# Kernel optimization log

Measured on AMD Instinct MI355X. Metric: run time of the kernel, lower is better.

The kernel has to match this reference:

```python
import jax, jax.numpy as jnp
import numpy as np

NUM_GROUPS = 32
EPS = 1e-5


def _conv(x, w, b, pad):
    # x: [B,C,H,W], w: [O,I,kh,kw]
    y = jax.lax.conv_general_dilated(
        x, w, window_strides=(1, 1), padding=[(pad, pad), (pad, pad)],
        dimension_numbers=('NCHW', 'OIHW', 'NCHW'))
    return y + b[None, :, None, None]


def _group_norm(x, gamma, beta):
    B, C, H, W = x.shape
    g = x.reshape(B, NUM_GROUPS, C // NUM_GROUPS, H, W)
    mu = g.mean(axis=(2, 3, 4), keepdims=True)
    var = g.var(axis=(2, 3, 4), keepdims=True)
    g = (g - mu) * jax.lax.rsqrt(var + EPS)
    x = g.reshape(B, C, H, W)
    return x * gamma[None, :, None, None] + beta[None, :, None, None]


def setup_inputs() -> dict:
    key = jax.random.key(0)
    ks = jax.random.split(key, 8)
    B, C, H, W = 8, 384, 64, 64
    s1 = 1.0 / np.sqrt(C)          # 1x1 conv fan-in
    s3 = 1.0 / np.sqrt(C * 9)      # 3x3 conv fan-in
    return {
        'x': jax.random.normal(ks[0], (B, C, H, W), dtype=jnp.float32),
        'gamma': jnp.ones((C,), dtype=jnp.float32),
        'beta': jnp.zeros((C,), dtype=jnp.float32),
        'wq': jax.random.normal(ks[1], (C, C, 1, 1), dtype=jnp.float32) * s1,
        'bq': jnp.zeros((C,), dtype=jnp.float32),
        'wk': jax.random.normal(ks[2], (C, C, 3, 3), dtype=jnp.float32) * s3,
        'bk': jnp.zeros((C,), dtype=jnp.float32),
        'wv': jax.random.normal(ks[3], (C, C, 1, 1), dtype=jnp.float32) * s1,
        'bv': jnp.zeros((C,), dtype=jnp.float32),
        'wf': jax.random.normal(ks[4], (C, C, 1, 1), dtype=jnp.float32) * s1,
        'bf': jnp.zeros((C,), dtype=jnp.float32),
        'k': 512,
    }


def reference(x, gamma, beta, wq, bq, wk, bk, wv, bv, wf, bf, k):
    B, C, H, W = x.shape
    xn = _group_norm(x, gamma, beta)
    q = _conv(xn, wq, bq, 0)
    kk = _conv(xn, wk, bk, 1)
    v = _conv(xn, wv, bv, 0)
    # frequency-domain correlation: elementwise product of 2D spectra
    Fq = jnp.fft.fft2(q)
    Fk = jnp.fft.fft2(kk)
    A = jnp.fft.ifft2(Fq * Fk).real          # [B,C,H,W]
    # per-(batch,channel) spatial top-k sparsification
    A_flat = A.reshape(B, C, H * W)
    topv, _ = jax.lax.top_k(A_flat, k)
    thresh = topv[..., -1:]                   # k-th largest value
    masked = jnp.where(A_flat >= thresh, A_flat, -jnp.inf)
    Fw = jax.nn.softmax(masked, axis=-1).reshape(B, C, H, W)
    F4 = v * Fw                               # weighted values
    res = _conv(F4, wf, bf, 0)
    return xn * res
```

## Files before the change

### kernel.cpp

```cpp
#include <hip/hip_runtime.h>
#include <hip/hip_fp16.h>
#include <math.h>

#define CCH  384
#define BATCH 8
#define HWN  4096
#define NG   32
#define CPG  12
#define KSEL 512
#define FFTP 65
#define LP   40

typedef short v8s  __attribute__((ext_vector_type(8)));
typedef float v16f __attribute__((ext_vector_type(16)));

#define MFMA_B16(A_,B_,C_) __builtin_amdgcn_mfma_f32_32x32x16_bf16((A_),(B_),(C_),0,0,0)

#define BARRIER_NODRAIN() asm volatile("s_waitcnt lgkmcnt(0)\n\ts_barrier" ::: "memory")
#define BARRIER_RAW() asm volatile("s_barrier" ::: "memory")

__device__ __forceinline__ v8s as_v8s(uint4 u) {
  union { uint4 u4; v8s v; } c; c.u4 = u; return c.v;
}
__device__ __forceinline__ unsigned br6(unsigned i) {
  return ((i&1u)<<5)|((i&2u)<<3)|((i&4u)<<1)|((i&8u)>>1)|((i&16u)>>3)|((i&32u)>>5);
}
__device__ __forceinline__ unsigned f2key(float f) {
  unsigned u = __float_as_uint(f);
  return (u & 0x80000000u) ? ~u : (u | 0x80000000u);
}
__device__ __forceinline__ float wave_max(float v) {
#pragma unroll
  for (int o = 32; o > 0; o >>= 1) v = fmaxf(v, __shfl_down(v, o, 64));
  return v;
}
__device__ __forceinline__ float wave_sum(float v) {
#pragma unroll
  for (int o = 32; o > 0; o >>= 1) v += __shfl_down(v, o, 64);
  return v;
}
__device__ __forceinline__ unsigned short bf16_rne(float f) {
  unsigned u = __float_as_uint(f);
  return (unsigned short)((u + 0x7fffu + ((u >> 16) & 1u)) >> 16);
}
__device__ __forceinline__ float bf2f(unsigned short h) {
  return __uint_as_float(((unsigned)h) << 16);
}

#define MFMA12_RR(a0h,a0l,a1h,a1l,b0h,b0l,b1h,b1l)            \
  __builtin_amdgcn_s_setprio(1);                              \
  acc[0][0] = MFMA_B16(a0h, b0h, acc[0][0]);                  \
  acc[0][1] = MFMA_B16(a0h, b1h, acc[0][1]);                  \
  acc[1][0] = MFMA_B16(a1h, b0h, acc[1][0]);                  \
  acc[1][1] = MFMA_B16(a1h, b1h, acc[1][1]);                  \
  acc[0][0] = MFMA_B16(a0h, b0l, acc[0][0]);                  \
  acc[0][1] = MFMA_B16(a0h, b1l, acc[0][1]);                  \
  acc[1][0] = MFMA_B16(a1h, b0l, acc[1][0]);                  \
  acc[1][1] = MFMA_B16(a1h, b1l, acc[1][1]);                  \
  acc[0][0] = MFMA_B16(a0l, b0h, acc[0][0]);                  \
  acc[0][1] = MFMA_B16(a0l, b1h, acc[0][1]);                  \
  acc[1][0] = MFMA_B16(a1l, b0h, acc[1][0]);                  \
  acc[1][1] = MFMA_B16(a1l, b1h, acc[1][1]);                  \
  __builtin_amdgcn_s_setprio(0);

__global__ __launch_bounds__(256) void stats_kernel(const float* __restrict__ x,
                                                    float2* __restrict__ gs,
                                                    unsigned short* __restrict__ zp) {
  int b = blockIdx.x >> 5, g = blockIdx.x & 31;
  if (blockIdx.x == 0 && threadIdx.x < 8) zp[threadIdx.x] = 0;
  size_t base = ((size_t)b * CCH + (size_t)g * CPG) * HWN;
  const float4* xp = (const float4*)(x + base);
  int tid = threadIdx.x;
  const int N4 = CPG * HWN / 4;
  float s = 0.f, ss = 0.f;
  for (int i = tid; i < N4; i += 256) {
    float4 v = xp[i];
    s  += (v.x + v.y) + (v.z + v.w);
    ss += (v.x*v.x + v.y*v.y) + (v.z*v.z + v.w*v.w);
  }
  s = wave_sum(s); ss = wave_sum(ss);
  __shared__ float sb[4], qb[4];
  if ((tid & 63) == 0) { sb[tid >> 6] = s; qb[tid >> 6] = ss; }
  __syncthreads();
  if (tid == 0) {
    float S = sb[0]+sb[1]+sb[2]+sb[3], Q = qb[0]+qb[1]+qb[2]+qb[3];
    float inv = 1.0f / (float)(CPG * HWN);
    float mu = S * inv;
    float var = Q * inv - mu * mu;
    gs[blockIdx.x] = make_float2(mu, rsqrtf(var + 1e-5f));
  }
}

__global__ __launch_bounds__(256) void pack_split_k(const float* __restrict__ w,
    unsigned short* __restrict__ hi, unsigned short* __restrict__ lo, int n) {
  int i = blockIdx.x * 256 + threadIdx.x;
  if (i >= n) return;
  float f = w[i];
  int m = i / 384, ci = i - m * 384;
  int kc = ci >> 4, tt = ci & 15;
  int mb = m >> 5, lm2 = m & 31;
  int l = ((tt >> 3) << 5) | lm2;
  int j = tt & 7;
  size_t o = (((size_t)kc * 12 + mb) << 9) + ((size_t)l << 3) + j;
  unsigned short h = bf16_rne(f);
  hi[o] = h;
  lo[o] = bf16_rne(f - bf2f(h));
}
__global__ __launch_bounds__(256) void pack9_k(const float* __restrict__ w,
    unsigned short* __restrict__ hi, unsigned short* __restrict__ lo) {
  int i = blockIdx.x * 256 + threadIdx.x;
  int r = blockIdx.y;
  float f = w[(size_t)i * 9 + r];
  int m = i / 384, ci = i - m * 384;
  int kc = ci >> 4, tt = ci & 15;
  int mb = m >> 5, lm2 = m & 31;
  int l = ((tt >> 3) << 5) | lm2;
  int j = tt & 7;
  size_t o = (((size_t)(r * 24 + kc) * 12 + mb) << 9) + ((size_t)l << 3) + j;
  unsigned short h = bf16_rne(f);
  hi[o] = h;
  lo[o] = bf16_rne(f - bf2f(h));
}

template<int FUSE, int SPLIT>
__global__ __launch_bounds__(256) void trans_kernel(const float* __restrict__ in,
    const float2* __restrict__ gs, const float* __restrict__ gamma,
    const float* __restrict__ beta,
    unsigned short* __restrict__ oh, unsigned short* __restrict__ ol) {
  __shared__ float ts[64][65];
  int tid = threadIdx.x;
  int b = blockIdx.z, c0 = blockIdx.y * 64, p0 = blockIdx.x * 64;
#pragma unroll
  for (int i = 0; i < 4; ++i) {
    int idx = tid + (i << 8);
    int row = idx >> 4, col = (idx & 15) << 2;
    float4 v = *(const float4*)&in[((size_t)b*CCH + c0 + row)*HWN + p0 + col];
    if (FUSE) {
      int c = c0 + row;
      float2 st = gs[(b << 5) + c / CPG];
      float a = gamma[c] * st.y, bb = beta[c] - st.x * a;
      v.x = v.x*a+bb; v.y = v.y*a+bb; v.z = v.z*a+bb; v.w = v.w*a+bb;
    }
    ts[row][col] = v.x; ts[row][col+1] = v.y; ts[row][col+2] = v.z; ts[row][col+3] = v.w;
  }
  __syncthreads();
#pragma unroll
  for (int i = 0; i < 2; ++i) {
    int idx = tid + (i << 8);
    int p = idx >> 3, cgp = (idx & 7) << 3;
    unsigned short h8[8] __attribute__((aligned(16)));
    unsigned short l8[8] __attribute__((aligned(16)));
#pragma unroll
    for (int j = 0; j < 8; ++j) {
      float f = ts[cgp + j][p];
      unsigned short hb = bf16_rne(f);
      h8[j] = hb;
      if (SPLIT) l8[j] = bf16_rne(f - bf2f(hb));
    }
    size_t o = ((size_t)b*HWN + p0 + p)*CCH + c0 + cgp;
    *(uint4*)&oh[o] = *(const uint4*)h8;
    if (SPLIT) *(uint4*)&ol[o] = *(const uint4*)l8;
  }
}

template<int TAPS, int OUT>
__global__ __launch_bounds__(256, 3) void mm_kernel(
    const unsigned short* __restrict__ Ahg, const unsigned short* __restrict__ Alg,
    const float* __restrict__ bias,
    const unsigned short* __restrict__ Bhg, const unsigned short* __restrict__ Blg,
    const unsigned short* __restrict__ xnTh, const unsigned short* __restrict__ xnTl,
    void* __restrict__ Yv) {
  __shared__ unsigned short Bh_s[2][128*LP], Bl_s[2][128*LP];
  int tid = threadIdx.x;
  int b = blockIdx.z, m0 = blockIdx.y * 128, n0 = blockIdx.x * 128;
  int y0 = blockIdx.x * 2;
  int u0row = tid >> 2, cg = tid & 3;
  int lds0 = u0row * LP + cg * 8, lds1 = lds0 + 64 * LP;
  int lane = tid & 63, wm = tid >> 7, wn = (tid >> 6) & 1;
  int lm = lane & 31, lh = lane >> 5;
  int brow = (wn * 64 + lm) * LP;
  int mbb = blockIdx.y * 4 + wm * 2;
  int laneoff = lane << 3;

  v16f acc[2][2];
#pragma unroll
  for (int t = 0; t < 2; ++t)
#pragma unroll
    for (int s = 0; s < 2; ++s)
#pragma unroll
      for (int g = 0; g < 16; ++g) acc[t][s][g] = 0.f;

  const int NS = TAPS * 12;
  uint4 rb0h, rb0l, rb1h, rb1l;
  uint4 rA0h_h0, rA0l_h0, rA1h_h0, rA1l_h0;
  uint4 rA0h_h1, rA0l_h1, rA1h_h1, rA1l_h1;

  auto issueB = [&](int s) {
    int c0 = s * 32;
    int px = u0row;
    int py0 = y0, py1 = py0 + 1;
    size_t boff0 = ((size_t)b * HWN + py0 * 64 + px) * CCH + cg * 8 + c0;
    size_t boff1 = ((size_t)b * HWN + py1 * 64 + px) * CCH + cg * 8 + c0;
    rb0h = *(const uint4*)(Bhg + boff0);
    rb0l = *(const uint4*)(Blg + boff0);
    rb1h = *(const uint4*)(Bhg + boff1);
    rb1l = *(const uint4*)(Blg + boff1);
  };
  auto loadA0 = [&](int s) {
    int fragcol = s * 2;
    size_t off = (((size_t)fragcol * 12 + mbb) << 9) + laneoff;
    rA0h_h0 = *(const uint4*)(Ahg + off);
    rA0l_h0 = *(const uint4*)(Alg + off);
    rA1h_h0 = *(const uint4*)(Ahg + off + 512);
    rA1l_h0 = *(const uint4*)(Alg + off + 512);
  };
  auto loadA1 = [&](int s) {
    int fragcol = s * 2 + 1;
    size_t off = (((size_t)fragcol * 12 + mbb) << 9) + laneoff;
    rA0h_h1 = *(const uint4*)(Ahg + off);
    rA0l_h1 = *(const uint4*)(Alg + off);
    rA1h_h1 = *(const uint4*)(Ahg + off + 512);
    rA1l_h1 = *(const uint4*)(Alg + off + 512);
  };

  issueB(0);
  loadA0(0); loadA1(0);
  *(uint4*)&Bh_s[0][lds0] = rb0h; *(uint4*)&Bl_s[0][lds0] = rb0l;
  *(uint4*)&Bh_s[0][lds1] = rb1h; *(uint4*)&Bl_s[0][lds1] = rb1l;
  issueB(1);
  BARRIER_NODRAIN();

  for (int s = 0; s < NS; ++s) {
    const int cur = s & 1;
    const unsigned short* Bh = &Bh_s[cur][0];
    const unsigned short* Bl = &Bl_s[cur][0];
    {
      int co = lh << 3;
      v8s b0h = *(const v8s*)&Bh[brow + co];
      v8s b0l = *(const v8s*)&Bl[brow + co];
      v8s b1h = *(const v8s*)&Bh[brow + 32*LP + co];
      v8s b1l = *(const v8s*)&Bl[brow + 32*LP + co];
      v8s a0h = as_v8s(rA0h_h0), a0l = as_v8s(rA0l_h0);
      v8s a1h = as_v8s(rA1h_h0), a1l = as_v8s(rA1l_h0);
      MFMA12_RR(a0h, a0l, a1h, a1l, b0h, b0l, b1h, b1l)
    }
    if (s + 1 < NS) loadA0(s + 1);
    {
      int co = 16 + (lh << 3);
      v8s b0h = *(const v8s*)&Bh[brow + co];
      v8s b0l = *(const v8s*)&Bl[brow + co];
      v8s b1h = *(const v8s*)&Bh[brow + 32*LP + co];
      v8s b1l = *(const v8s*)&Bl[brow + 32*LP + co];
      v8s a0h = as_v8s(rA0h_h1), a0l = as_v8s(rA0l_h1);
      v8s a1h = as_v8s(rA1h_h1), a1l = as_v8s(rA1l_h1);
      MFMA12_RR(a0h, a0l, a1h, a1l, b0h, b0l, b1h, b1l)
    }
    if (s + 1 < NS) {
      loadA1(s + 1);
      int nxt = cur ^ 1;
      *(uint4*)&Bh_s[nxt][lds0] = rb0h; *(uint4*)&Bl_s[nxt][lds0] = rb0l;
      *(uint4*)&Bh_s[nxt][lds1] = rb1h; *(uint4*)&Bl_s[nxt][lds1] = rb1l;
      if (s + 2 < NS) issueB(s + 2);
      BARRIER_NODRAIN();
    }
  }
#pragma unroll
  for (int t = 0; t < 2; ++t) {
    int mb = m0 + wm * 64 + t * 32;
#pragma unroll
    for (int s = 0; s < 2; ++s) {
      int n = n0 + wn * 64 + s * 32 + lm;
#pragma unroll
      for (int g = 0; g < 16; ++g) {
        int m = mb + (g & 3) + ((g >> 2) << 3) + (lh << 2);
        float val = acc[t][s][g] + bias[m];
        size_t oidx = ((size_t)b * CCH + m) * HWN + n;
        if (OUT == 0) {
          ((float*)Yv)[oidx] = val;
        } else if (OUT == 1) {
          ((__half*)Yv)[oidx] = __float2half(val);
        } else {
          size_t tix = ((size_t)b * HWN + n) * CCH + m;
          float xnv = bf2f(xnTh[tix]) + bf2f(xnTl[tix]);
          ((float*)Yv)[oidx] = val * xnv;
        }
      }
    }
  }
}

__global__ __launch_bounds__(256, 3) void mm9_kernel(
    const unsigned short* __restrict__ Ahg, const unsigned short* __restrict__ Alg,
    const float* __restrict__ bias,
    const unsigned short* __restrict__ Bhg, const unsigned short* __restrict__ Blg,
    const unsigned short* __restrict__ zp,
    float* __restrict__ Y) {
  __shared__ unsigned short Bh_s[2*66*LP], Bl_s[2*66*LP];
  int tid = threadIdx.x;
  int b = blockIdx.z, m0 = blockIdx.y * 128, n0 = blockIdx.x * 128;
  int y0 = blockIdx.x * 2;
  int lane = tid & 63, wm = tid >> 7, wn = (tid >> 6) & 1;
  int lm = lane & 31, lh = lane >> 5;
  int mbb = blockIdx.y * 4 + wm * 2;
  int laneoff = lane << 3;
  const int b0i = (wn * 66 + lm + 1) * LP + lh * 8;

  v16f acc[2][2];
#pragma unroll
  for (int t = 0; t < 2; ++t)
#pragma unroll
    for (int s = 0; s < 2; ++s)
#pragma unroll
      for (int g = 0; g < 16; ++g) acc[t][s][g] = 0.f;

  if (tid < 128) {
    int py = (tid >> 6) & 1, e = (tid >> 5) & 1, ch = tid & 31;
    int px = e ? 65 : 0;
    Bh_s[(py*66 + px)*LP + ch] = 0;
    Bl_s[(py*66 + px)*LP + ch] = 0;
  }

  uint4 rs0, rs1, rs2, rs3;
  auto issueSlab = [&](int si2) {
    int dyi2 = si2 / 12, cidx2 = si2 - dyi2 * 12;
    int dy = dyi2 - 1;
#pragma unroll
    for (int k2 = 0; k2 < 4; ++k2) {
      int cid = tid + (k2 << 8);
      int rr = cid & 511;
      int py = rr >> 8;
      int r3 = rr & 255;
      int px0 = r3 >> 2, cs = r3 & 3;
      int pyi = y0 + dy + py;
      bool ok = (unsigned)pyi < 64u;
      size_t go = ok ? (((size_t)b * HWN + pyi * 64 + px0) * CCH + cidx2 * 32 + cs * 8) : 0;
      const unsigned short* src = (cid < 512) ? (ok ? Bhg + go : zp)
                                              : (ok ? Blg + go : zp);
      uint4 v = *(const uint4*)src;
      if (k2 == 0) rs0 = v; else if (k2 == 1) rs1 = v;
      else if (k2 == 2) rs2 = v; else rs3 = v;
    }
  };
  auto writeSlab = [&]() {
#pragma unroll
    for (int k2 = 0; k2 < 4; ++k2) {
      int cid = tid + (k2 << 8);
      int rr = cid & 511;
      int py = rr >> 8;
      int r3 = rr & 255;
      int px0 = r3 >> 2, cs = r3 & 3;
      int dst = (py * 66 + px0 + 1) * LP + cs * 8;
      unsigned short* arr = (cid < 512) ? Bh_s : Bl_s;
      uint4 v = (k2 == 0) ? rs0 : (k2 == 1) ? rs1 : (k2 == 2) ? rs2 : rs3;
      *(uint4*)&arr[dst] = v;
    }
  };

  uint4 rA0h_h0, rA0l_h0, rA1h_h0, rA1l_h0;
  uint4 rA0h_h1, rA0l_h1, rA1h_h1, rA1l_h1;
  auto loadAh0 = [&](int fragcol) {
    size_t off = (((size_t)fragcol * 12 + mbb) << 9) + laneoff;
    rA0h_h0 = *(const uint4*)(Ahg + off);
    rA0l_h0 = *(const uint4*)(Alg + off);
    rA1h_h0 = *(const uint4*)(Ahg + off + 512);
    rA1l_h0 = *(const uint4*)(Alg + off + 512);
  };
  auto loadAh1 = [&](int fragcol) {
    size_t off = (((size_t)(fragcol + 1) * 12 + mbb) << 9) + laneoff;
    rA0h_h1 = *(const uint4*)(Ahg + off);
    rA0l_h1 = *(const uint4*)(Alg + off);
    rA1h_h1 = *(const uint4*)(Ahg + off + 512);
    rA1l_h1 = *(const uint4*)(Alg + off + 512);
  };
  auto ldSo = [&](const unsigned short* arr, int cofs) -> v8s {
    return *(const v8s*)&arr[b0i + cofs];
  };

  issueSlab(0);
  writeSlab();
  issueSlab(1);
  loadAh0(0);
  loadAh1(0);
  __syncthreads();

  int dyi = 0, cidx = 0;
  for (int si = 0; si < 36; ++si) {
    int rbase = dyi * 3;
    int ndyi = (cidx == 11) ? dyi + 1 : dyi;
    int ncidx = (cidx == 11) ? 0 : cidx + 1;
#pragma unroll
    for (int dxi = 0; dxi < 3; ++dxi) {
      const int dx = dxi - 1;
      bool last = (si == 35) && (dxi == 2);
      int nfc = (dxi < 2) ? ((rbase + dxi + 1) * 24 + cidx * 2)
                          : ((ndyi * 3) * 24 + ncidx * 2);
      {
        v8s b0h = ldSo(Bh_s, dx * LP),             b1h = ldSo(Bh_s, (32 + dx) * LP);
        v8s b0l = ldSo(Bl_s, dx * LP),             b1l = ldSo(Bl_s, (32 + dx) * LP);
        v8s a0h = as_v8s(rA0h_h0), a0l = as_v8s(rA0l_h0);
        v8s a1h = as_v8s(rA1h_h0), a1l = as_v8s(rA1l_h0);
        MFMA12_RR(a0h, a0l, a1h, a1l, b0h, b0l, b1h, b1l)
      }
      if (!last) loadAh0(nfc);
      {
        v8s b0h = ldSo(Bh_s, dx * LP + 16),        b1h = ldSo(Bh_s, (32 + dx) * LP + 16);
        v8s b0l = ldSo(Bl_s, dx * LP + 16),        b1l = ldSo(Bl_s, (32 + dx) * LP + 16);
        v8s a0h = as_v8s(rA0h_h1), a0l = as_v8s(rA0l_h1);
        v8s a1h = as_v8s(rA1h_h1), a1l = as_v8s(rA1l_h1);
        MFMA12_RR(a0h, a0l, a1h, a1l, b0h, b0l, b1h, b1l)
      }
      if (!last) loadAh1(nfc);
    }
    if (si < 35) {
      BARRIER_RAW();
      writeSlab();
      if (si + 2 < 36) issueSlab(si + 2);
      BARRIER_NODRAIN();
    }
    dyi = ndyi; cidx = ncidx;
  }

#pragma unroll
  for (int t = 0; t < 2; ++t) {
    int mb = m0 + wm * 64 + t * 32;
#pragma unroll
    for (int s = 0; s < 2; ++s) {
      int n = n0 + wn * 64 + s * 32 + lm;
#pragma unroll
      for (int g = 0; g < 16; ++g) {
        int m = mb + (g & 3) + ((g >> 2) << 3) + (lh << 2);
        Y[((size_t)b * CCH + m) * HWN + n] = acc[t][s][g] + bias[m];
      }
    }
  }
}

__device__ __forceinline__ void fft4_pass(float* zr, float* zi,
    const float* twr, const float* twi, int tid, int axis, float ds) {
#pragma unroll
  for (int s = 0; s < 3; ++s) {
    const int h = 1 << (2 * s);
#pragma unroll
    for (int tt = 0; tt < 4; ++tt) {
      int t = tid + (tt << 8);
      int line = t >> 4, bf = t & 15;
      int j  = bf & (h - 1);
      int i0 = ((bf >> (2 * s)) << (2 * s + 2)) + j;
      int e1 = j << (5 - 2 * s);
      int e2 = j << (4 - 2 * s);
      float w1r = twr[e1], w1i = ds * twi[e1];
      float w2r = twr[e2], w2i = ds * twi[e2];
      int A0, st;
      if (axis == 0) { A0 = line * FFTP + i0; st = h; }
      else           { A0 = i0 * FFTP + line; st = h * FFTP; }
      int A1 = A0 + st, A2 = A1 + st, A3 = A2 + st;
      float x0r = zr[A0], x0i = zi[A0];
      float x1r = zr[A1], x1i = zi[A1];
      float x2r = zr[A2], x2i = zi[A2];
      float x3r = zr[A3], x3i = zi[A3];
      float t1r = x1r*w1r - x1i*w1i, t1i = x1r*w1i + x1i*w1r;
      float t3r = x3r*w1r - x3i*w1i, t3i = x3r*w1i + x3i*w1r;
      float u0r = x0r + t1r, u0i = x0i + t1i;
      float u1r = x0r - t1r, u1i = x0i - t1i;
      float u2r = x2r + t3r, u2i = x2i + t3i;
      float u3r = x2r - t3r, u3i = x2i - t3i;
      float c2r = u2r*w2r - u2i*w2i, c2i = u2r*w2i + u2i*w2r;
      float c3r = u3r*w2r - u3i*w2i, c3i = u3r*w2i + u3i*w2r;
      zr[A0] = u0r + c2r;      zi[A0] = u0i + c2i;
      zr[A2] = u0r - c2r;      zi[A2] = u0i - c2i;
      zr[A1] = u1r + ds*c3i;   zi[A1] = u1i - ds*c3r;
      zr[A3] = u1r - ds*c3i;   zi[A3] = u1i + ds*c3r;
    }
    __syncthreads();
  }
}

__global__ __launch_bounds__(256) void fft_topk_kernel(
    const float* q, const float* __restrict__ kkb,
    const __half* __restrict__ v, float* F4) {
  __shared__ float zr[64 * FFTP], zi[64 * FFTP];
  __shared__ float twr[32], twi[32];
  __shared__ unsigned hist[4][256];
  __shared__ unsigned su2[2];
  __shared__ unsigned wtot[4];
  __shared__ float sred[5];
  int tid = threadIdx.x;
  int lane = tid & 63, w = tid >> 6;
  size_t base = (size_t)blockIdx.x * HWN;
  for (int i = tid; i < HWN; i += 256) {
    int y = i >> 6, x = i & 63;
    int slot = br6(y) * FFTP + br6(x);
    zr[slot] = q[base + i];
    zi[slot] = kkb[base + i];
  }
  if (tid < 32) {
    float ang = (float)tid * 0.0981747704246810387f;
    twr[tid] = cosf(ang);
    twi[tid] = -sinf(ang);
  }
  __syncthreads();
  fft4_pass(zr, zi, twr, twi, tid, 0, 1.f);
  fft4_pass(zr, zi, twr, twi, tid, 1, 1.f);
  float prr[16], pir[16];
#pragma unroll
  for (int c = 0; c < 16; c++) {
    int i = tid + (c << 8);
    int ky = i >> 6, kx = i & 63;
    float sr = zr[ky * FFTP + kx], si = zi[ky * FFTP + kx];
    int kyn = (64 - ky) & 63, kxn = (64 - kx) & 63;
    float nr = zr[kyn * FFTP + kxn], ni = zi[kyn * FFTP + kxn];
    float fqr = 0.5f * (sr + nr), fqi = 0.5f * (si - ni);
    float fkr = 0.5f * (si + ni), fki = 0.5f * (nr - sr);
    prr[c] = fqr * fkr - fqi * fki;
    pir[c] = fqr * fki + fqi * fkr;
  }
  __syncthreads();
#pragma unroll
  for (int c = 0; c < 16; c++) {
    int i = tid + (c << 8);
    int ky = i >> 6, kx = i & 63;
    int slot = br6(ky) * FFTP + br6(kx);
    zr[slot] = prr[c];
    zi[slot] = pir[c];
  }
  __syncthreads();
  fft4_pass(zr, zi, twr, twi, tid, 0, -1.f);
  fft4_pass(zr, zi, twr, twi, tid, 1, -1.f);
  const float scale = 1.0f / 4096.0f;
  float a[16];
  unsigned key[16];
  float mx = -3.0e38f;
#pragma unroll
  for (int c = 0; c < 16; c++) {
    int i = tid + (c << 8);
    a[c] = zr[(i >> 6) * FFTP + (i & 63)] * scale;
    key[c] = f2key(a[c]);
    mx = fmaxf(mx, a[c]);
  }
  mx = wave_max(mx);
  if (lane == 0) sred[w] = mx;
  __syncthreads();
  if (tid == 0) sred[4] = fmaxf(fmaxf(sred[0], sred[1]), fmaxf(sred[2], sred[3]));
  __syncthreads();
  float am = sred[4];
  unsigned prefix = 0; int kr = KSEL;
  for (int pass = 0; pass < 4; pass++) {
    int shift = 24 - (pass << 3);
#pragma unroll
    for (int ww = 0; ww < 4; ++ww) hist[ww][tid] = 0;
    __syncthreads();
#pragma unroll
    for (int c = 0; c < 16; c++) {
      unsigned u = key[c];
      if (((u ^ prefix) >> shift) <= 0xFFu)
        atomicAdd(&hist[w][(u >> shift) & 255u], 1u);
    }
    __syncthreads();
    unsigned xv = hist[0][tid] + hist[1][tid] + hist[2][tid] + hist[3][tid];
#pragma unroll
    for (int o = 1; o < 64; o <<= 1) {
      unsigned t2 = __shfl_down(xv, o, 64);
      if (lane + o < 64) xv += t2;
    }
    if (lane == 0) wtot[w] = xv;
    __syncthreads();
    for (int ww = w + 1; ww < 4; ++ww) xv += wtot[ww];
    hist[0][tid] = xv;
    __syncthreads();
    unsigned sv = xv;
    unsigned svn = (tid < 255) ? hist[0][tid + 1] : 0u;
    if (sv >= (unsigned)kr && svn < (unsigned)kr) { su2[0] = (unsigned)tid; su2[1] = svn; }
    __syncthreads();
    prefix |= su2[0] << shift;
    kr -= (int)su2[1];
  }
  unsigned thr = prefix;
  float lsum = 0.f;
#pragma unroll
  for (int c = 0; c < 16; c++) {
    float e = (key[c] >= thr) ? __expf(a[c] - am) : 0.f;
    a[c] = e;
    lsum += e;
  }
  lsum = wave_sum(lsum);
  if (lane == 0) sred[w] = lsum;
  __syncthreads();
  if (tid == 0) sred[4] = 1.0f / (sred[0] + sred[1] + sred[2] + sred[3]);
  __syncthreads();
  float inv = sred[4];
#pragma unroll
  for (int c = 0; c < 16; c++) {
    int i = tid + (c << 8);
    F4[base + i] = __half2float(v[base + i]) * (a[c] * inv);
  }
}

extern "C" void kernel_launch(void* const* d_in, const int* in_sizes, int n_in,
                              void* d_out, int out_size, void* d_ws, size_t ws_size,
                              hipStream_t stream) {
  const float* x     = (const float*)d_in[0];
  const float* gamma = (const float*)d_in[1];
  const float* beta  = (const float*)d_in[2];
  const float* wq    = (const float*)d_in[3];
  const float* bq    = (const float*)d_in[4];
  const float* wk    = (const float*)d_in[5];
  const float* bk    = (const float*)d_in[6];
  const float* wv    = (const float*)d_in[7];
  const float* bv    = (const float*)d_in[8];
  const float* wf    = (const float*)d_in[9];
  const float* bf    = (const float*)d_in[10];

  const size_t NEL = (size_t)BATCH * CCH * HWN;
  const size_t WSZ = (size_t)CCH * CCH;

  unsigned short* xnTh = (unsigned short*)d_ws;
  unsigned short* xnTl = xnTh + NEL;
  float*  qC  = (float*)(xnTl + NEL);
  float*  kD  = qC + NEL;
  __half* vE  = (__half*)(kD + NEL);
  unsigned short* W = (unsigned short*)(vE + NEL);
  unsigned short* Wqh = W;
  unsigned short* Wql = Wqh + WSZ;
  unsigned short* Wvh = Wql + WSZ;
  unsigned short* Wvl = Wvh + WSZ;
  unsigned short* Wfh = Wvl + WSZ;
  unsigned short* Wfl = Wfh + WSZ;
  unsigned short* Wkh = Wfl + WSZ;
  unsigned short* Wkl = Wkh + 9 * WSZ;
  float2* gs = (float2*)(Wkl + 9 * WSZ);
  unsigned short* zp = (unsigned short*)(gs + BATCH * NG);
  unsigned short* F4Th = (unsigned short*)kD;
  unsigned short* F4Tl = F4Th + NEL;

  pack_split_k<<<dim3(576), dim3(256), 0, stream>>>(wq, Wqh, Wql, (int)WSZ);
  pack_split_k<<<dim3(576), dim3(256), 0, stream>>>(wv, Wvh, Wvl, (int)WSZ);
  pack_split_k<<<dim3(576), dim3(256), 0, stream>>>(wf, Wfh, Wfl, (int)WSZ);
  pack9_k<<<dim3(576, 9), dim3(256), 0, stream>>>(wk, Wkh, Wkl);
  stats_kernel<<<dim3(BATCH * NG), dim3(256), 0, stream>>>(x, gs, zp);
  trans_kernel<1, 1><<<dim3(64, 6, BATCH), dim3(256), 0, stream>>>(
      x, gs, gamma, beta, xnTh, xnTl);

  dim3 gm(32, 3, BATCH);
  mm_kernel<1, 0><<<gm, dim3(256), 0, stream>>>(Wqh, Wql, bq, xnTh, xnTl,
                                                nullptr, nullptr, qC);
  mm9_kernel<<<gm, dim3(256), 0, stream>>>(Wkh, Wkl, bk, xnTh, xnTl, zp, kD);
  mm_kernel<1, 1><<<gm, dim3(256), 0, stream>>>(Wvh, Wvl, bv, xnTh, xnTl,
                                                nullptr, nullptr, vE);

  fft_topk_kernel<<<dim3(BATCH * CCH), dim3(256), 0, stream>>>(qC, kD, vE, qC);

  trans_kernel<0, 1><<<dim3(64, 6, BATCH), dim3(256), 0, stream>>>(
      qC, nullptr, nullptr, nullptr, F4Th, F4Tl);

  mm_kernel<1, 2><<<gm, dim3(256), 0, stream>>>(Wfh, Wfl, bf, F4Th, F4Tl,
                                                xnTh, xnTl, d_out);
}
```

Measured before the change: 671.0 us.

## Halve GEMM N-tile to 64 and recompute softmax exponentials

The 1x1 and 3x3 split-bf16 GEMM kernels move from 128x128 to 128x64 output tiles. This halves accumulators, LDS buffers and B-slab loads per block, and doubles the grid with a higher occupancy hint of 4 blocks per CU. The aim is more parallelism and latency hiding, at the cost of less B reuse per A fragment and more A traffic. The top-k softmax kernel now recomputes the exponentials in the write loop instead of keeping them in registers, trading extra exp work for lower register pressure.

```diff
diff --git a/kernel.cpp b/kernel.cpp
--- a/kernel.cpp
+++ b/kernel.cpp
@@ -46,22 +46,6 @@
 __device__ __forceinline__ float bf2f(unsigned short h) {
   return __uint_as_float(((unsigned)h) << 16);
 }
-
-#define MFMA12_RR(a0h,a0l,a1h,a1l,b0h,b0l,b1h,b1l)            \
-  __builtin_amdgcn_s_setprio(1);                              \
-  acc[0][0] = MFMA_B16(a0h, b0h, acc[0][0]);                  \
-  acc[0][1] = MFMA_B16(a0h, b1h, acc[0][1]);                  \
-  acc[1][0] = MFMA_B16(a1h, b0h, acc[1][0]);                  \
-  acc[1][1] = MFMA_B16(a1h, b1h, acc[1][1]);                  \
-  acc[0][0] = MFMA_B16(a0h, b0l, acc[0][0]);                  \
-  acc[0][1] = MFMA_B16(a0h, b1l, acc[0][1]);                  \
-  acc[1][0] = MFMA_B16(a1h, b0l, acc[1][0]);                  \
-  acc[1][1] = MFMA_B16(a1h, b1l, acc[1][1]);                  \
-  acc[0][0] = MFMA_B16(a0l, b0h, acc[0][0]);                  \
-  acc[0][1] = MFMA_B16(a0l, b1h, acc[0][1]);                  \
-  acc[1][0] = MFMA_B16(a1l, b0h, acc[1][0]);                  \
-  acc[1][1] = MFMA_B16(a1l, b1h, acc[1][1]);                  \
-  __builtin_amdgcn_s_setprio(0);
 
 __global__ __launch_bounds__(256) void stats_kernel(const float* __restrict__ x,
                                                     float2* __restrict__ gs,
@@ -164,47 +148,39 @@
 }
 
 template<int TAPS, int OUT>
-__global__ __launch_bounds__(256, 3) void mm_kernel(
+__global__ __launch_bounds__(256, 4) void mm_kernel(
     const unsigned short* __restrict__ Ahg, const unsigned short* __restrict__ Alg,
     const float* __restrict__ bias,
     const unsigned short* __restrict__ Bhg, const unsigned short* __restrict__ Blg,
     const unsigned short* __restrict__ xnTh, const unsigned short* __restrict__ xnTl,
     void* __restrict__ Yv) {
-  __shared__ unsigned short Bh_s[2][128*LP], Bl_s[2][128*LP];
+  __shared__ unsigned short Bh_s[2][64*LP], Bl_s[2][64*LP];
   int tid = threadIdx.x;
-  int b = blockIdx.z, m0 = blockIdx.y * 128, n0 = blockIdx.x * 128;
-  int y0 = blockIdx.x * 2;
+  int b = blockIdx.z, m0 = blockIdx.y * 128;
+  int n0 = blockIdx.x << 6;
   int u0row = tid >> 2, cg = tid & 3;
-  int lds0 = u0row * LP + cg * 8, lds1 = lds0 + 64 * LP;
+  int lds0 = u0row * LP + cg * 8;
   int lane = tid & 63, wm = tid >> 7, wn = (tid >> 6) & 1;
   int lm = lane & 31, lh = lane >> 5;
-  int brow = (wn * 64 + lm) * LP;
+  int brow = (wn * 32 + lm) * LP;
   int mbb = blockIdx.y * 4 + wm * 2;
   int laneoff = lane << 3;
 
-  v16f acc[2][2];
+  v16f acc[2];
 #pragma unroll
   for (int t = 0; t < 2; ++t)
 #pragma unroll
-    for (int s = 0; s < 2; ++s)
-#pragma unroll
-      for (int g = 0; g < 16; ++g) acc[t][s][g] = 0.f;
-
-  const int NS = TAPS * 12;
-  uint4 rb0h, rb0l, rb1h, rb1l;
+    for (int g = 0; g < 16; ++g) acc[t][g] = 0.f;
+
+  const int NS = 12;
+  uint4 rbh, rbl;
   uint4 rA0h_h0, rA0l_h0, rA1h_h0, rA1l_h0;
   uint4 rA0h_h1, rA0l_h1, rA1h_h1, rA1l_h1;
 
   auto issueB = [&](int s) {
-    int c0 = s * 32;
-    int px = u0row;
-    int py0 = y0, py1 = py0 + 1;
-    size_t boff0 = ((size_t)b * HWN + py0 * 64 + px) * CCH + cg * 8 + c0;
-    size_t boff1 = ((size_t)b * HWN + py1 * 64 + px) * CCH + cg * 8 + c0;
-    rb0h = *(const uint4*)(Bhg + boff0);
-    rb0l = *(const uint4*)(Blg + boff0);
-    rb1h = *(const uint4*)(Bhg + boff1);
-    rb1l = *(const uint4*)(Blg + boff1);
+    size_t boff = ((size_t)b * HWN + n0 + u0row) * CCH + cg * 8 + s * 32;
+    rbh = *(const uint4*)(Bhg + boff);
+    rbl = *(const uint4*)(Blg + boff);
   };
   auto loadA0 = [&](int s) {
     int fragcol = s * 2;
@@ -225,8 +201,7 @@
 
   issueB(0);
   loadA0(0); loadA1(0);
-  *(uint4*)&Bh_s[0][lds0] = rb0h; *(uint4*)&Bl_s[0][lds0] = rb0l;
-  *(uint4*)&Bh_s[0][lds1] = rb1h; *(uint4*)&Bl_s[0][lds1] = rb1l;
+  *(uint4*)&Bh_s[0][lds0] = rbh; *(uint4*)&Bl_s[0][lds0] = rbl;
   issueB(1);
   BARRIER_NODRAIN();
 
@@ -238,28 +213,37 @@
       int co = lh << 3;
       v8s b0h = *(const v8s*)&Bh[brow + co];
       v8s b0l = *(const v8s*)&Bl[brow + co];
-      v8s b1h = *(const v8s*)&Bh[brow + 32*LP + co];
-      v8s b1l = *(const v8s*)&Bl[brow + 32*LP + co];
       v8s a0h = as_v8s(rA0h_h0), a0l = as_v8s(rA0l_h0);
       v8s a1h = as_v8s(rA1h_h0), a1l = as_v8s(rA1l_h0);
-      MFMA12_RR(a0h, a0l, a1h, a1l, b0h, b0l, b1h, b1l)
+      __builtin_amdgcn_s_setprio(1);
+      acc[0] = MFMA_B16(a0h, b0h, acc[0]);
+      acc[0] = MFMA_B16(a0h, b0l, acc[0]);
+      acc[0] = MFMA_B16(a0l, b0h, acc[0]);
+      acc[1] = MFMA_B16(a1h, b0h, acc[1]);
+      acc[1] = MFMA_B16(a1h, b0l, acc[1]);
+      acc[1] = MFMA_B16(a1l, b0h, acc[1]);
+      __builtin_amdgcn_s_setprio(0);
     }
     if (s + 1 < NS) loadA0(s + 1);
     {
       int co = 16 + (lh << 3);
       v8s b0h = *(const v8s*)&Bh[brow + co];
       v8s b0l = *(const v8s*)&Bl[brow + co];
-      v8s b1h = *(const v8s*)&Bh[brow + 32*LP + co];
-      v8s b1l = *(const v8s*)&Bl[brow + 32*LP + co];
       v8s a0h = as_v8s(rA0h_h1), a0l = as_v8s(rA0l_h1);
       v8s a1h = as_v8s(rA1h_h1), a1l = as_v8s(rA1l_h1);
-      MFMA12_RR(a0h, a0l, a1h, a1l, b0h, b0l, b1h, b1l)
+      __builtin_amdgcn_s_setprio(1);
+      acc[0] = MFMA_B16(a0h, b0h, acc[0]);
+      acc[0] = MFMA_B16(a0h, b0l, acc[0]);
+      acc[0] = MFMA_B16(a0l, b0h, acc[0]);
+      acc[1] = MFMA_B16(a1h, b0h, acc[1]);
+      acc[1] = MFMA_B16(a1h, b0l, acc[1]);
+      acc[1] = MFMA_B16(a1l, b0h, acc[1]);
+      __builtin_amdgcn_s_setprio(0);
     }
     if (s + 1 < NS) {
       loadA1(s + 1);
       int nxt = cur ^ 1;
-      *(uint4*)&Bh_s[nxt][lds0] = rb0h; *(uint4*)&Bl_s[nxt][lds0] = rb0l;
-      *(uint4*)&Bh_s[nxt][lds1] = rb1h; *(uint4*)&Bl_s[nxt][lds1] = rb1l;
+      *(uint4*)&Bh_s[nxt][lds0] = rbh; *(uint4*)&Bl_s[nxt][lds0] = rbl;
       if (s + 2 < NS) issueB(s + 2);
       BARRIER_NODRAIN();
     }
@@ -267,93 +251,67 @@
 #pragma unroll
   for (int t = 0; t < 2; ++t) {
     int mb = m0 + wm * 64 + t * 32;
-#pragma unroll
-    for (int s = 0; s < 2; ++s) {
-      int n = n0 + wn * 64 + s * 32 + lm;
-#pragma unroll
-      for (int g = 0; g < 16; ++g) {
-        int m = mb + (g & 3) + ((g >> 2) << 3) + (lh << 2);
-        float val = acc[t][s][g] + bias[m];
-        size_t oidx = ((size_t)b * CCH + m) * HWN + n;
-        if (OUT == 0) {
-          ((float*)Yv)[oidx] = val;
-        } else if (OUT == 1) {
-          ((__half*)Yv)[oidx] = __float2half(val);
-        } else {
-          size_t tix = ((size_t)b * HWN + n) * CCH + m;
-          float xnv = bf2f(xnTh[tix]) + bf2f(xnTl[tix]);
-          ((float*)Yv)[oidx] = val * xnv;
-        }
+    int n = n0 + wn * 32 + lm;
+#pragma unroll
+    for (int g = 0; g < 16; ++g) {
+      int m = mb + (g & 3) + ((g >> 2) << 3) + (lh << 2);
+      float val = acc[t][g] + bias[m];
+      size_t oidx = ((size_t)b * CCH + m) * HWN + n;
+      if (OUT == 0) {
+        ((float*)Yv)[oidx] = val;
+      } else if (OUT == 1) {
+        ((__half*)Yv)[oidx] = __float2half(val);
+      } else {
+        size_t tix = ((size_t)b * HWN + n) * CCH + m;
+        float xnv = bf2f(xnTh[tix]) + bf2f(xnTl[tix]);
+        ((float*)Yv)[oidx] = val * xnv;
       }
     }
   }
 }
 
-__global__ __launch_bounds__(256, 3) void mm9_kernel(
+__global__ __launch_bounds__(256, 4) void mm9_kernel(
     const unsigned short* __restrict__ Ahg, const unsigned short* __restrict__ Alg,
     const float* __restrict__ bias,
     const unsigned short* __restrict__ Bhg, const unsigned short* __restrict__ Blg,
     const unsigned short* __restrict__ zp,
     float* __restrict__ Y) {
-  __shared__ unsigned short Bh_s[2*66*LP], Bl_s[2*66*LP];
+  __shared__ unsigned short Bh_s[66*LP], Bl_s[66*LP];
   int tid = threadIdx.x;
-  int b = blockIdx.z, m0 = blockIdx.y * 128, n0 = blockIdx.x * 128;
-  int y0 = blockIdx.x * 2;
+  int b = blockIdx.z, m0 = blockIdx.y * 128;
+  int y0 = blockIdx.x;
+  int n0 = y0 << 6;
   int lane = tid & 63, wm = tid >> 7, wn = (tid >> 6) & 1;
   int lm = lane & 31, lh = lane >> 5;
   int mbb = blockIdx.y * 4 + wm * 2;
   int laneoff = lane << 3;
-  const int b0i = (wn * 66 + lm + 1) * LP + lh * 8;
-
-  v16f acc[2][2];
+
+  v16f acc[2];
 #pragma unroll
   for (int t = 0; t < 2; ++t)
 #pragma unroll
-    for (int s = 0; s < 2; ++s)
-#pragma unroll
-      for (int g = 0; g < 16; ++g) acc[t][s][g] = 0.f;
+    for (int g = 0; g < 16; ++g) acc[t][g] = 0.f;
 
   if (tid < 128) {
-    int py = (tid >> 6) & 1, e = (tid >> 5) & 1, ch = tid & 31;
-    int px = e ? 65 : 0;
-    Bh_s[(py*66 + px)*LP + ch] = 0;
-    Bl_s[(py*66 + px)*LP + ch] = 0;
-  }
-
-  uint4 rs0, rs1, rs2, rs3;
+    int ch = tid & 31;
+    int px = ((tid >> 5) & 1) ? 65 : 0;
+    if (tid < 64) Bh_s[px * LP + ch] = 0; else Bl_s[px * LP + ch] = 0;
+  }
+
+  uint4 rs0, rs1;
+  int px0s = tid >> 2, css = tid & 3;
   auto issueSlab = [&](int si2) {
     int dyi2 = si2 / 12, cidx2 = si2 - dyi2 * 12;
-    int dy = dyi2 - 1;
-#pragma unroll
-    for (int k2 = 0; k2 < 4; ++k2) {
-      int cid = tid + (k2 << 8);
-      int rr = cid & 511;
-      int py = rr >> 8;
-      int r3 = rr & 255;
-      int px0 = r3 >> 2, cs = r3 & 3;
-      int pyi = y0 + dy + py;
-      bool ok = (unsigned)pyi < 64u;
-      size_t go = ok ? (((size_t)b * HWN + pyi * 64 + px0) * CCH + cidx2 * 32 + cs * 8) : 0;
-      const unsigned short* src = (cid < 512) ? (ok ? Bhg + go : zp)
-                                              : (ok ? Blg + go : zp);
-      uint4 v = *(const uint4*)src;
-      if (k2 == 0) rs0 = v; else if (k2 == 1) rs1 = v;
-      else if (k2 == 2) rs2 = v; else rs3 = v;
-    }
+    int pyi = y0 + dyi2 - 1;
+    bool ok = (unsigned)pyi < 64u;
+    size_t go = ok ? (((size_t)b * HWN + pyi * 64 + px0s) * CCH + cidx2 * 32 + css * 8) : 0;
+    rs0 = *(const uint4*)(ok ? Bhg + go : zp);
+    rs1 = *(const uint4*)(ok ? Blg + go : zp);
   };
   auto writeSlab = [&]() {
-#pragma unroll
-    for (int k2 = 0; k2 < 4; ++k2) {
-      int cid = tid + (k2 << 8);
-      int rr = cid & 511;
-      int py = rr >> 8;
-      int r3 = rr & 255;
-      int px0 = r3 >> 2, cs = r3 & 3;
-      int dst = (py * 66 + px0 + 1) * LP + cs * 8;
-      unsigned short* arr = (cid < 512) ? Bh_s : Bl_s;
-      uint4 v = (k2 == 0) ? rs0 : (k2 == 1) ? rs1 : (k2 == 2) ? rs2 : rs3;
-      *(uint4*)&arr[dst] = v;
-    }
+    int dst = (px0s + 1) * LP + css * 8;
+    *(uint4*)&Bh_s[dst] = rs0;
+    *(uint4*)&Bl_s[dst] = rs1;
   };
 
   uint4 rA0h_h0, rA0l_h0, rA1h_h0, rA1l_h0;
@@ -372,8 +330,9 @@
     rA1h_h1 = *(const uint4*)(Ahg + off + 512);
     rA1l_h1 = *(const uint4*)(Alg + off + 512);
   };
-  auto ldSo = [&](const unsigned short* arr, int cofs) -> v8s {
-    return *(const v8s*)&arr[b0i + cofs];
+  auto ldS = [&](const unsigned short* base, int h, int dx) -> v8s {
+    int px = wn * 32 + lm + dx + 1;
+    return *(const v8s*)&base[px * LP + h * 16 + lh * 8];
   };
 
   issueSlab(0);
@@ -395,19 +354,33 @@
       int nfc = (dxi < 2) ? ((rbase + dxi + 1) * 24 + cidx * 2)
                           : ((ndyi * 3) * 24 + ncidx * 2);
       {
-        v8s b0h = ldSo(Bh_s, dx * LP),             b1h = ldSo(Bh_s, (32 + dx) * LP);
-        v8s b0l = ldSo(Bl_s, dx * LP),             b1l = ldSo(Bl_s, (32 + dx) * LP);
+        v8s b0h = ldS(Bh_s, 0, dx);
+        v8s b0l = ldS(Bl_s, 0, dx);
         v8s a0h = as_v8s(rA0h_h0), a0l = as_v8s(rA0l_h0);
         v8s a1h = as_v8s(rA1h_h0), a1l = as_v8s(rA1l_h0);
-        MFMA12_RR(a0h, a0l, a1h, a1l, b0h, b0l, b1h, b1l)
+        __builtin_amdgcn_s_setprio(1);
+        acc[0] = MFMA_B16(a0h, b0h, acc[0]);
+        acc[0] = MFMA_B16(a0h, b0l, acc[0]);
+        acc[0] = MFMA_B16(a0l, b0h, acc[0]);
+        acc[1] = MFMA_B16(a1h, b0h, acc[1]);
+        acc[1] = MFMA_B16(a1h, b0l, acc[1]);
+        acc[1] = MFMA_B16(a1l, b0h, acc[1]);
+        __builtin_amdgcn_s_setprio(0);
       }
       if (!last) loadAh0(nfc);
       {
-        v8s b0h = ldSo(Bh_s, dx * LP + 16),        b1h = ldSo(Bh_s, (32 + dx) * LP + 16);
-        v8s b0l = ldSo(Bl_s, dx * LP + 16),        b1l = ldSo(Bl_s, (32 + dx) * LP + 16);
+        v8s b0h = ldS(Bh_s, 1, dx);
+        v8s b0l = ldS(Bl_s, 1, dx);
         v8s a0h = as_v8s(rA0h_h1), a0l = as_v8s(rA0l_h1);
         v8s a1h = as_v8s(rA1h_h1), a1l = as_v8s(rA1l_h1);
-        MFMA12_RR(a0h, a0l, a1h, a1l, b0h, b0l, b1h, b1l)
+        __builtin_amdgcn_s_setprio(1);
+        acc[0] = MFMA_B16(a0h, b0h, acc[0]);
+        acc[0] = MFMA_B16(a0h, b0l, acc[0]);
+        acc[0] = MFMA_B16(a0l, b0h, acc[0]);
+        acc[1] = MFMA_B16(a1h, b0h, acc[1]);
+        acc[1] = MFMA_B16(a1h, b0l, acc[1]);
+        acc[1] = MFMA_B16(a1l, b0h, acc[1]);
+        __builtin_amdgcn_s_setprio(0);
       }
       if (!last) loadAh1(nfc);
     }
@@ -423,14 +396,11 @@
 #pragma unroll
   for (int t = 0; t < 2; ++t) {
     int mb = m0 + wm * 64 + t * 32;
-#pragma unroll
-    for (int s = 0; s < 2; ++s) {
-      int n = n0 + wn * 64 + s * 32 + lm;
-#pragma unroll
-      for (int g = 0; g < 16; ++g) {
-        int m = mb + (g & 3) + ((g >> 2) << 3) + (lh << 2);
-        Y[((size_t)b * CCH + m) * HWN + n] = acc[t][s][g] + bias[m];
-      }
+    int n = n0 + wn * 32 + lm;
+#pragma unroll
+    for (int g = 0; g < 16; ++g) {
+      int m = mb + (g & 3) + ((g >> 2) << 3) + (lh << 2);
+      Y[((size_t)b * CCH + m) * HWN + n] = acc[t][g] + bias[m];
     }
   }
 }
@@ -577,11 +547,8 @@
   unsigned thr = prefix;
   float lsum = 0.f;
 #pragma unroll
-  for (int c = 0; c < 16; c++) {
-    float e = (key[c] >= thr) ? __expf(a[c] - am) : 0.f;
-    a[c] = e;
-    lsum += e;
-  }
+  for (int c = 0; c < 16; c++)
+    if (key[c] >= thr) lsum += expf(a[c] - am);
   lsum = wave_sum(lsum);
   if (lane == 0) sred[w] = lsum;
   __syncthreads();
@@ -591,7 +558,8 @@
 #pragma unroll
   for (int c = 0; c < 16; c++) {
     int i = tid + (c << 8);
-    F4[base + i] = __half2float(v[base + i]) * (a[c] * inv);
+    float wgt = (key[c] >= thr) ? expf(a[c] - am) * inv : 0.f;
+    F4[base + i] = __half2float(v[base + i]) * wgt;
   }
 }
 
@@ -640,7 +608,7 @@
   trans_kernel<1, 1><<<dim3(64, 6, BATCH), dim3(256), 0, stream>>>(
       x, gs, gamma, beta, xnTh, xnTl);
 
-  dim3 gm(32, 3, BATCH);
+  dim3 gm(64, 3, BATCH);
   mm_kernel<1, 0><<<gm, dim3(256), 0, stream>>>(Wqh, Wql, bq, xnTh, xnTl,
                                                 nullptr, nullptr, qC);
   mm9_kernel<<<gm, dim3(256), 0, stream>>>(Wkh, Wkl, bk, xnTh, xnTl, zp, kD);
```

After: 680.3 us. About the same (+1.4%).
